# Optimization experiments

Hardware: AMD Instinct MI355X
Metric: run time of the kernel (lower is better)

## Reference

```python
import jax, jax.numpy as jnp
import numpy as np

N_NODES = 100000
N_EDGES = 600000
F_IN = 128
F_OUT = 128


def setup_inputs() -> dict:
    key = jax.random.key(0)
    ks = jax.random.split(key, 9)
    stdv = 1.0 / np.sqrt(F_OUT)
    return {
        "x": jax.random.normal(ks[0], (N_NODES, F_IN), dtype=jnp.float32),
        "weight": jax.random.uniform(ks[1], (F_IN, F_OUT), dtype=jnp.float32, minval=-stdv, maxval=stdv),
        "bias": jax.random.uniform(ks[2], (F_OUT,), dtype=jnp.float32, minval=-stdv, maxval=stdv),
        "vals0": jax.random.uniform(ks[3], (N_EDGES,), dtype=jnp.float32),
        "vals1": jax.random.uniform(ks[4], (N_EDGES,), dtype=jnp.float32),
        "rows0": jax.random.randint(ks[5], (N_EDGES,), 0, N_NODES, dtype=jnp.int32),
        "cols0": jax.random.randint(ks[6], (N_EDGES,), 0, N_NODES, dtype=jnp.int32),
        "rows1": jax.random.randint(ks[7], (N_EDGES,), 0, N_NODES, dtype=jnp.int32),
        "cols1": jax.random.randint(ks[8], (N_EDGES,), 0, N_NODES, dtype=jnp.int32),
    }


def _spmm(rows, cols, vals, dense, n):
    # COO sparse [n,n] @ dense [n,f]: gather source rows, scale, scatter-add to dest rows
    msgs = dense[cols] * vals[:, None]          # [E, f]
    return jax.ops.segment_sum(msgs, rows, num_segments=n)


def reference(x, weight, bias, vals0, vals1, rows0, cols0, rows1, cols1):
    n = x.shape[0]
    support = x @ weight                         # [N, F_OUT] dense GEMM
    out = _spmm(rows0, cols0, vals0, support, n) \
        + _spmm(rows1, cols1, vals1, support, n)
    return out + bias
```

## Files before the change

### kernel.cpp

```cpp
#include <hip/hip_runtime.h>


#define FDIM 128
#define EPB 2048

typedef __attribute__((ext_vector_type(8))) short short8;
typedef __attribute__((ext_vector_type(4))) float floatx4;

__device__ __forceinline__ unsigned short f32_to_bf16(float f) {
    unsigned int u = __float_as_uint(f);
    unsigned int r = u + 0x7fffu + ((u >> 16) & 1u);
    return (unsigned short)(r >> 16);
}

__device__ __forceinline__ float bf16_lo(unsigned int u) {
    return __uint_as_float((u & 0xffffu) << 16);
}
__device__ __forceinline__ float bf16_hi(unsigned int u) {
    return __uint_as_float(u & 0xffff0000u);
}

__global__ __launch_bounds__(256) void wt_conv(const float* __restrict__ w,
                                               unsigned short* __restrict__ wt) {
    int idx = blockIdx.x * 256 + threadIdx.x;
    int nn = idx >> 7, k = idx & 127;
    wt[idx] = f32_to_bf16(w[(size_t)k * FDIM + nn]);
}

__global__ __launch_bounds__(256) void gemm_reg(const float* __restrict__ x,
                                                const unsigned short* __restrict__ wt,
                                                unsigned short* __restrict__ support,
                                                int n) {
    const int tid = threadIdx.x;
    const int wv = tid >> 6, lane = tid & 63;
    const int quad = lane >> 4, lr = lane & 15;
    const int row0 = (blockIdx.x * 4 + wv) * 16;
    if (row0 >= n) return;

    short8 b[8][4];
    #pragma unroll
    for (int nt = 0; nt < 8; ++nt)
        #pragma unroll
        for (int ks = 0; ks < 4; ++ks)
            b[nt][ks] = *(const short8*)(wt + (size_t)(nt * 16 + lr) * FDIM + ks * 32 + quad * 8);

    floatx4 acc[8];
    #pragma unroll
    for (int nt = 0; nt < 8; ++nt) acc[nt] = (floatx4)0.f;

    const int arow = row0 + lr;
    const bool rowok = arow < n;
    const float* xr = x + (size_t)arow * FDIM;

    float4 f[8];
    #pragma unroll
    for (int ks = 0; ks < 4; ++ks) {
        f[2 * ks]     = rowok ? *(const float4*)(xr + ks * 32 + quad * 8)     : make_float4(0.f,0.f,0.f,0.f);
        f[2 * ks + 1] = rowok ? *(const float4*)(xr + ks * 32 + quad * 8 + 4) : make_float4(0.f,0.f,0.f,0.f);
    }

    #pragma unroll
    for (int ks = 0; ks < 4; ++ks) {
        float4 lo = f[2 * ks], hi = f[2 * ks + 1];
        short8 a;
        a[0] = (short)f32_to_bf16(lo.x); a[1] = (short)f32_to_bf16(lo.y);
        a[2] = (short)f32_to_bf16(lo.z); a[3] = (short)f32_to_bf16(lo.w);
        a[4] = (short)f32_to_bf16(hi.x); a[5] = (short)f32_to_bf16(hi.y);
        a[6] = (short)f32_to_bf16(hi.z); a[7] = (short)f32_to_bf16(hi.w);
        #pragma unroll
        for (int nt = 0; nt < 8; ++nt)
            acc[nt] = __builtin_amdgcn_mfma_f32_16x16x32_bf16(a, b[nt][ks], acc[nt], 0, 0, 0);
    }

    #pragma unroll
    for (int i = 0; i < 4; ++i) {
        int row = row0 + quad * 4 + i;
        if (row < n) {
            #pragma unroll
            for (int nt = 0; nt < 8; ++nt)
                support[(size_t)row * FDIM + nt * 16 + lr] = f32_to_bf16(acc[nt][i]);
        }
    }
}

__global__ __launch_bounds__(256) void hist_rows(const int* __restrict__ rows0,
                                                 const int* __restrict__ rows1,
                                                 int* __restrict__ count,
                                                 int* __restrict__ rank, int E) {
    int gid = blockIdx.x * 256 + threadIdx.x;
    if (gid >= 2 * E) return;
    int r = (gid < E) ? rows0[gid] : rows1[gid - E];
    rank[gid] = atomicAdd(&count[r], 1);
}

__device__ __forceinline__ int block_incl_scan(int v, int tid, int* lds) {
    int lane = tid & 63, wv = tid >> 6;
    #pragma unroll
    for (int d = 1; d < 64; d <<= 1) {
        int y = __shfl_up(v, d);
        if (lane >= d) v += y;
    }
    if (lane == 63) lds[wv] = v;
    __syncthreads();
    if (wv == 0 && lane < 4) {
        int s = lds[lane];
        #pragma unroll
        for (int d = 1; d < 4; d <<= 1) {
            int y = __shfl_up(s, d);
            if (lane >= d) s += y;
        }
        lds[4 + lane] = s;
    }
    __syncthreads();
    int add = (wv > 0) ? lds[4 + wv - 1] : 0;
    return v + add;
}

__global__ __launch_bounds__(256) void rowptr_scan(const int* __restrict__ count,
                                                   int* __restrict__ rowptr,
                                                   int* __restrict__ gcur, int n) {
    __shared__ int lds[8];
    __shared__ int base;
    int tid = threadIdx.x;
    int idx = blockIdx.x * 256 + tid;
    int v = (idx < n) ? count[idx] : 0;
    int inc = block_incl_scan(v, tid, lds);
    if (tid == 255) base = atomicAdd(gcur, inc);
    __syncthreads();
    if (idx < n) rowptr[idx] = base + inc - v;
}

__global__ __launch_bounds__(256) void compute_pos(const int* __restrict__ rows0,
                                                   const int* __restrict__ rows1,
                                                   const int* __restrict__ rank,
                                                   const int* __restrict__ rowptr,
                                                   int* __restrict__ pos, int E) {
    int gid = blockIdx.x * 256 + threadIdx.x;
    if (gid >= 2 * E) return;
    int r = (gid < E) ? rows0[gid] : rows1[gid - E];
    pos[gid] = rowptr[r] + rank[gid];
}

__global__ __launch_bounds__(256) void scatter_pos(
    const int* __restrict__ cols0, const float* __restrict__ vals0,
    const int* __restrict__ cols1, const float* __restrict__ vals1,
    const int* __restrict__ pos,
    int2* __restrict__ rec, int E, int psize) {
    const int p = blockIdx.x & 7;
    const int base = (blockIdx.x >> 3) * EPB;
    const int tid = threadIdx.x;
    #pragma unroll
    for (int it = 0; it < EPB / 256; ++it) {
        int gid = base + it * 256 + tid;
        if (gid < 2 * E) {
            int pv = pos[gid];
            if (pv / psize == p) {
                int c; float v;
                if (gid < E) { c = cols0[gid]; v = vals0[gid]; }
                else         { int e = gid - E; c = cols1[e]; v = vals1[e]; }
                rec[pv] = make_int2(c, __float_as_int(v));
            }
        }
    }
}

__global__ __launch_bounds__(256) void pull_csr(const unsigned short* __restrict__ support,
                                                const int* __restrict__ rowptr,
                                                const int* __restrict__ count,
                                                const int2* __restrict__ rec,
                                                const float* __restrict__ bias,
                                                float* __restrict__ out, int n) {
    int wid = (blockIdx.x * 256 + threadIdx.x) >> 6;
    int lane = threadIdx.x & 63;
    if (wid >= n) return;
    int beg = rowptr[wid];
    int end = beg + count[wid];
    float ax = 0.f, ay = 0.f;
    const char* sp = (const char*)support;
    const unsigned loff = (unsigned)lane << 2;

    for (int base = beg; base < end; base += 64) {
        int m = end - base; if (m > 64) m = 64;
        long long pk = 0;
        if (lane < m) pk = *(const long long*)&rec[base + lane];
        int j = 0;
        for (; j + 8 <= m; j += 8) {
            long long p0 = __shfl(pk, j);
            long long p1 = __shfl(pk, j + 1);
            long long p2 = __shfl(pk, j + 2);
            long long p3 = __shfl(pk, j + 3);
            long long p4 = __shfl(pk, j + 4);
            long long p5 = __shfl(pk, j + 5);
            long long p6 = __shfl(pk, j + 6);
            long long p7 = __shfl(pk, j + 7);
            unsigned u0 = *(const unsigned*)(sp + (((unsigned)p0) << 8) + loff);
            unsigned u1 = *(const unsigned*)(sp + (((unsigned)p1) << 8) + loff);
            unsigned u2 = *(const unsigned*)(sp + (((unsigned)p2) << 8) + loff);
            unsigned u3 = *(const unsigned*)(sp + (((unsigned)p3) << 8) + loff);
            unsigned u4 = *(const unsigned*)(sp + (((unsigned)p4) << 8) + loff);
            unsigned u5 = *(const unsigned*)(sp + (((unsigned)p5) << 8) + loff);
            unsigned u6 = *(const unsigned*)(sp + (((unsigned)p6) << 8) + loff);
            unsigned u7 = *(const unsigned*)(sp + (((unsigned)p7) << 8) + loff);
            float v0 = __int_as_float((int)(p0 >> 32));
            float v1 = __int_as_float((int)(p1 >> 32));
            float v2 = __int_as_float((int)(p2 >> 32));
            float v3 = __int_as_float((int)(p3 >> 32));
            float v4 = __int_as_float((int)(p4 >> 32));
            float v5 = __int_as_float((int)(p5 >> 32));
            float v6 = __int_as_float((int)(p6 >> 32));
            float v7 = __int_as_float((int)(p7 >> 32));
            ax += v0 * bf16_lo(u0); ay += v0 * bf16_hi(u0);
            ax += v1 * bf16_lo(u1); ay += v1 * bf16_hi(u1);
            ax += v2 * bf16_lo(u2); ay += v2 * bf16_hi(u2);
            ax += v3 * bf16_lo(u3); ay += v3 * bf16_hi(u3);
            ax += v4 * bf16_lo(u4); ay += v4 * bf16_hi(u4);
            ax += v5 * bf16_lo(u5); ay += v5 * bf16_hi(u5);
            ax += v6 * bf16_lo(u6); ay += v6 * bf16_hi(u6);
            ax += v7 * bf16_lo(u7); ay += v7 * bf16_hi(u7);
        }
        for (; j + 4 <= m; j += 4) {
            long long p0 = __shfl(pk, j);
            long long p1 = __shfl(pk, j + 1);
            long long p2 = __shfl(pk, j + 2);
            long long p3 = __shfl(pk, j + 3);
            unsigned u0 = *(const unsigned*)(sp + (((unsigned)p0) << 8) + loff);
            unsigned u1 = *(const unsigned*)(sp + (((unsigned)p1) << 8) + loff);
            unsigned u2 = *(const unsigned*)(sp + (((unsigned)p2) << 8) + loff);
            unsigned u3 = *(const unsigned*)(sp + (((unsigned)p3) << 8) + loff);
            float v0 = __int_as_float((int)(p0 >> 32));
            float v1 = __int_as_float((int)(p1 >> 32));
            float v2 = __int_as_float((int)(p2 >> 32));
            float v3 = __int_as_float((int)(p3 >> 32));
            ax += v0 * bf16_lo(u0); ay += v0 * bf16_hi(u0);
            ax += v1 * bf16_lo(u1); ay += v1 * bf16_hi(u1);
            ax += v2 * bf16_lo(u2); ay += v2 * bf16_hi(u2);
            ax += v3 * bf16_lo(u3); ay += v3 * bf16_hi(u3);
        }
        for (; j < m; ++j) {
            long long p = __shfl(pk, j);
            unsigned u = *(const unsigned*)(sp + (((unsigned)p) << 8) + loff);
            float v = __int_as_float((int)(p >> 32));
            ax += v * bf16_lo(u); ay += v * bf16_hi(u);
        }
    }
    float2 b = *(const float2*)(bias + lane * 2);
    *(float2*)(out + (size_t)wid * FDIM + lane * 2) = make_float2(ax + b.x, ay + b.y);
}

__global__ __launch_bounds__(256) void init_bias(const float* __restrict__ bias,
                                                 float* __restrict__ out, int n) {
    int idx = blockIdx.x * 256 + threadIdx.x;
    int total = n * (FDIM / 4);
    if (idx < total) {
        int j = (idx & (FDIM / 4 - 1)) * 4;
        float4 b = *(const float4*)(bias + j);
        *(float4*)(out + (size_t)idx * 4) = b;
    }
}

__global__ __launch_bounds__(256) void scatter_bf16(
    const unsigned short* __restrict__ support,
    const int* __restrict__ rows0, const int* __restrict__ cols0, const float* __restrict__ vals0,
    const int* __restrict__ rows1, const int* __restrict__ cols1, const float* __restrict__ vals1,
    float* __restrict__ out, int E) {
    int gid = blockIdx.x * 256 + threadIdx.x;
    int lane = gid & 63;
    int eg = gid >> 6;
    if (eg >= 2 * E) return;
    int r, c; float v;
    if (eg < E) { r = rows0[eg]; c = cols0[eg]; v = vals0[eg]; }
    else        { int e = eg - E; r = rows1[e]; c = cols1[e]; v = vals1[e]; }
    unsigned int u = *(const unsigned int*)(support + (size_t)c * FDIM + lane * 2);
    float sx = bf16_lo(u);
    float sy = bf16_hi(u);
    float* op = out + (size_t)r * FDIM + lane * 2;
    atomicAdd(op,     sx * v);
    atomicAdd(op + 1, sy * v);
}

static inline size_t align256(size_t v) { return (v + 255) & ~(size_t)255; }

extern "C" void kernel_launch(void* const* d_in, const int* in_sizes, int n_in,
                              void* d_out, int out_size, void* d_ws, size_t ws_size,
                              hipStream_t stream) {
    const float* x     = (const float*)d_in[0];
    const float* w     = (const float*)d_in[1];
    const float* bias  = (const float*)d_in[2];
    const float* vals0 = (const float*)d_in[3];
    const float* vals1 = (const float*)d_in[4];
    const int*   rows0 = (const int*)d_in[5];
    const int*   cols0 = (const int*)d_in[6];
    const int*   rows1 = (const int*)d_in[7];
    const int*   cols1 = (const int*)d_in[8];
    const int n = in_sizes[0] / FDIM;
    const int E = in_sizes[3];
    float* out = (float*)d_out;

    const int NB = (n + 255) / 256;

    size_t off = 0;
    unsigned short* support = (unsigned short*)((char*)d_ws + off);
    off = align256(off + (size_t)n * FDIM * 2);
    unsigned short* wt = (unsigned short*)((char*)d_ws + off);
    off = align256(off + (size_t)FDIM * FDIM * 2);
    size_t count_off = off;
    int*  count  = (int*)((char*)d_ws + off);  off = align256(off + (size_t)n * 4);
    int*  gcur   = (int*)((char*)d_ws + off);  off = align256(off + 4);
    size_t zero_bytes = off - count_off;
    int*  rowptr = (int*)((char*)d_ws + off);  off = align256(off + (size_t)n * 4);
    int*  rank   = (int*)((char*)d_ws + off);  off = align256(off + (size_t)2 * E * 4);
    int*  pos    = (int*)((char*)d_ws + off);  off = align256(off + (size_t)2 * E * 4);
    int2* rec    = (int2*)((char*)d_ws + off); off = align256(off + (size_t)2 * E * 8);

    wt_conv<<<(FDIM * FDIM) / 256, 256, 0, stream>>>(w, wt);
    gemm_reg<<<(n + 63) / 64, 256, 0, stream>>>(x, wt, support, n);

    if (off <= ws_size) {
        hipMemsetAsync((char*)d_ws + count_off, 0, zero_bytes, stream);
        int eb = (2 * E + 255) / 256;
        hist_rows<<<eb, 256, 0, stream>>>(rows0, rows1, count, rank, E);
        rowptr_scan<<<NB, 256, 0, stream>>>(count, rowptr, gcur, n);
        compute_pos<<<eb, 256, 0, stream>>>(rows0, rows1, rank, rowptr, pos, E);
        int psize = (2 * E + 7) / 8;
        int ntiles = (2 * E + EPB - 1) / EPB;
        scatter_pos<<<ntiles * 8, 256, 0, stream>>>(cols0, vals0, cols1, vals1,
                                                    pos, rec, E, psize);
        pull_csr<<<(n + 3) / 4, 256, 0, stream>>>(support, rowptr, count, rec, bias, out, n);
    } else {
        int total4 = n * (FDIM / 4);
        init_bias<<<(total4 + 255) / 256, 256, 0, stream>>>(bias, out, n);
        long long tthreads = 2LL * E * 64;
        int blocks = (int)((tthreads + 255) / 256);
        scatter_bf16<<<blocks, 256, 0, stream>>>(support, rows0, cols0, vals0,
                                                 rows1, cols1, vals1, out, E);
    }
}
```

Before: 291.7 us.

## Fuse launches: merge weight prep with memset, GEMM with histogram, drop pos pass

Weight transpose/convert and the count zeroing now share one prep kernel, replacing a separate memset. The histogram blocks are appended to the GEMM grid, so the atomic counting runs alongside the MFMA work, and each GEMM wave now handles four 16-row tiles so the B fragments loaded into registers are reused. The compute_pos kernel and the pos array are removed: the scatter partitions by row and computes the destination from rowptr and rank directly. This cuts kernel launches and one full pass over the edges, at the cost of extra gathers in the scatter and a GEMM grid with fewer blocks.

```diff
diff --git a/kernel.cpp b/kernel.cpp
--- a/kernel.cpp
+++ b/kernel.cpp
@@ -20,22 +20,42 @@
     return __uint_as_float(u & 0xffff0000u);
 }
 
-__global__ __launch_bounds__(256) void wt_conv(const float* __restrict__ w,
-                                               unsigned short* __restrict__ wt) {
-    int idx = blockIdx.x * 256 + threadIdx.x;
-    int nn = idx >> 7, k = idx & 127;
-    wt[idx] = f32_to_bf16(w[(size_t)k * FDIM + nn]);
-}
-
-__global__ __launch_bounds__(256) void gemm_reg(const float* __restrict__ x,
-                                                const unsigned short* __restrict__ wt,
-                                                unsigned short* __restrict__ support,
-                                                int n) {
+__global__ __launch_bounds__(256) void prep(const float* __restrict__ w,
+                                            unsigned short* __restrict__ wt,
+                                            int* __restrict__ zero_ptr, int zero_ints) {
+    int bid = blockIdx.x;
+    if (bid < 64) {
+        int idx = bid * 256 + threadIdx.x;
+        int nn = idx >> 7, k = idx & 127;
+        wt[idx] = f32_to_bf16(w[(size_t)k * FDIM + nn]);
+    } else {
+        int idx = (bid - 64) * 256 + threadIdx.x;
+        if (idx < zero_ints) zero_ptr[idx] = 0;
+    }
+}
+
+__global__ __launch_bounds__(256) void gemm_hist(const float* __restrict__ x,
+                                                 const unsigned short* __restrict__ wt,
+                                                 unsigned short* __restrict__ support,
+                                                 int n,
+                                                 const int* __restrict__ rows0,
+                                                 const int* __restrict__ rows1,
+                                                 int* __restrict__ count,
+                                                 int* __restrict__ rank,
+                                                 int E, int GB) {
+    if ((int)blockIdx.x >= GB) {
+        int gid = (blockIdx.x - GB) * 256 + threadIdx.x;
+        if (gid < 2 * E) {
+            int r = (gid < E) ? rows0[gid] : rows1[gid - E];
+            rank[gid] = atomicAdd(&count[r], 1);
+        }
+        return;
+    }
     const int tid = threadIdx.x;
     const int wv = tid >> 6, lane = tid & 63;
     const int quad = lane >> 4, lr = lane & 15;
-    const int row0 = (blockIdx.x * 4 + wv) * 16;
-    if (row0 >= n) return;
+    const int rbase = blockIdx.x * 256 + wv * 64;
+    if (rbase >= n) return;
 
     short8 b[8][4];
     #pragma unroll
@@ -44,53 +64,41 @@
         for (int ks = 0; ks < 4; ++ks)
             b[nt][ks] = *(const short8*)(wt + (size_t)(nt * 16 + lr) * FDIM + ks * 32 + quad * 8);
 
-    floatx4 acc[8];
-    #pragma unroll
-    for (int nt = 0; nt < 8; ++nt) acc[nt] = (floatx4)0.f;
-
-    const int arow = row0 + lr;
-    const bool rowok = arow < n;
-    const float* xr = x + (size_t)arow * FDIM;
-
-    float4 f[8];
-    #pragma unroll
-    for (int ks = 0; ks < 4; ++ks) {
-        f[2 * ks]     = rowok ? *(const float4*)(xr + ks * 32 + quad * 8)     : make_float4(0.f,0.f,0.f,0.f);
-        f[2 * ks + 1] = rowok ? *(const float4*)(xr + ks * 32 + quad * 8 + 4) : make_float4(0.f,0.f,0.f,0.f);
-    }
-
-    #pragma unroll
-    for (int ks = 0; ks < 4; ++ks) {
-        float4 lo = f[2 * ks], hi = f[2 * ks + 1];
-        short8 a;
-        a[0] = (short)f32_to_bf16(lo.x); a[1] = (short)f32_to_bf16(lo.y);
-        a[2] = (short)f32_to_bf16(lo.z); a[3] = (short)f32_to_bf16(lo.w);
-        a[4] = (short)f32_to_bf16(hi.x); a[5] = (short)f32_to_bf16(hi.y);
-        a[6] = (short)f32_to_bf16(hi.z); a[7] = (short)f32_to_bf16(hi.w);
-        #pragma unroll
-        for (int nt = 0; nt < 8; ++nt)
-            acc[nt] = __builtin_amdgcn_mfma_f32_16x16x32_bf16(a, b[nt][ks], acc[nt], 0, 0, 0);
-    }
-
-    #pragma unroll
-    for (int i = 0; i < 4; ++i) {
-        int row = row0 + quad * 4 + i;
-        if (row < n) {
+    for (int t = 0; t < 4; ++t) {
+        const int row0 = rbase + t * 16;
+        if (row0 >= n) break;
+        const int arow = row0 + lr;
+        const bool rowok = arow < n;
+        const float* xr = x + (size_t)arow * FDIM;
+
+        floatx4 acc[8];
+        #pragma unroll
+        for (int nt = 0; nt < 8; ++nt) acc[nt] = (floatx4)0.f;
+
+        #pragma unroll
+        for (int ks = 0; ks < 4; ++ks) {
+            float4 lo = rowok ? *(const float4*)(xr + ks * 32 + quad * 8)     : make_float4(0.f,0.f,0.f,0.f);
+            float4 hi = rowok ? *(const float4*)(xr + ks * 32 + quad * 8 + 4) : make_float4(0.f,0.f,0.f,0.f);
+            short8 a;
+            a[0] = (short)f32_to_bf16(lo.x); a[1] = (short)f32_to_bf16(lo.y);
+            a[2] = (short)f32_to_bf16(lo.z); a[3] = (short)f32_to_bf16(lo.w);
+            a[4] = (short)f32_to_bf16(hi.x); a[5] = (short)f32_to_bf16(hi.y);
+            a[6] = (short)f32_to_bf16(hi.z); a[7] = (short)f32_to_bf16(hi.w);
             #pragma unroll
             for (int nt = 0; nt < 8; ++nt)
-                support[(size_t)row * FDIM + nt * 16 + lr] = f32_to_bf16(acc[nt][i]);
-        }
-    }
-}
-
-__global__ __launch_bounds__(256) void hist_rows(const int* __restrict__ rows0,
-                                                 const int* __restrict__ rows1,
-                                                 int* __restrict__ count,
-                                                 int* __restrict__ rank, int E) {
-    int gid = blockIdx.x * 256 + threadIdx.x;
-    if (gid >= 2 * E) return;
-    int r = (gid < E) ? rows0[gid] : rows1[gid - E];
-    rank[gid] = atomicAdd(&count[r], 1);
+                acc[nt] = __builtin_amdgcn_mfma_f32_16x16x32_bf16(a, b[nt][ks], acc[nt], 0, 0, 0);
+        }
+
+        #pragma unroll
+        for (int i = 0; i < 4; ++i) {
+            int row = row0 + quad * 4 + i;
+            if (row < n) {
+                #pragma unroll
+                for (int nt = 0; nt < 8; ++nt)
+                    support[(size_t)row * FDIM + nt * 16 + lr] = f32_to_bf16(acc[nt][i]);
+            }
+        }
+    }
 }
 
 __device__ __forceinline__ int block_incl_scan(int v, int tid, int* lds) {
@@ -130,22 +138,11 @@
     if (idx < n) rowptr[idx] = base + inc - v;
 }
 
-__global__ __launch_bounds__(256) void compute_pos(const int* __restrict__ rows0,
-                                                   const int* __restrict__ rows1,
-                                                   const int* __restrict__ rank,
-                                                   const int* __restrict__ rowptr,
-                                                   int* __restrict__ pos, int E) {
-    int gid = blockIdx.x * 256 + threadIdx.x;
-    if (gid >= 2 * E) return;
-    int r = (gid < E) ? rows0[gid] : rows1[gid - E];
-    pos[gid] = rowptr[r] + rank[gid];
-}
-
-__global__ __launch_bounds__(256) void scatter_pos(
-    const int* __restrict__ cols0, const float* __restrict__ vals0,
-    const int* __restrict__ cols1, const float* __restrict__ vals1,
-    const int* __restrict__ pos,
-    int2* __restrict__ rec, int E, int psize) {
+__global__ __launch_bounds__(256) void scatter_row(
+    const int* __restrict__ rows0, const int* __restrict__ cols0, const float* __restrict__ vals0,
+    const int* __restrict__ rows1, const int* __restrict__ cols1, const float* __restrict__ vals1,
+    const int* __restrict__ rank, const int* __restrict__ rowptr,
+    int2* __restrict__ rec, int E, int nper) {
     const int p = blockIdx.x & 7;
     const int base = (blockIdx.x >> 3) * EPB;
     const int tid = threadIdx.x;
@@ -153,12 +150,12 @@
     for (int it = 0; it < EPB / 256; ++it) {
         int gid = base + it * 256 + tid;
         if (gid < 2 * E) {
-            int pv = pos[gid];
-            if (pv / psize == p) {
+            int r = (gid < E) ? rows0[gid] : rows1[gid - E];
+            if (r / nper == p) {
                 int c; float v;
                 if (gid < E) { c = cols0[gid]; v = vals0[gid]; }
                 else         { int e = gid - E; c = cols1[e]; v = vals1[e]; }
-                rec[pv] = make_int2(c, __float_as_int(v));
+                rec[rowptr[r] + rank[gid]] = make_int2(c, __float_as_int(v));
             }
         }
     }
@@ -309,22 +306,26 @@
     size_t zero_bytes = off - count_off;
     int*  rowptr = (int*)((char*)d_ws + off);  off = align256(off + (size_t)n * 4);
     int*  rank   = (int*)((char*)d_ws + off);  off = align256(off + (size_t)2 * E * 4);
-    int*  pos    = (int*)((char*)d_ws + off);  off = align256(off + (size_t)2 * E * 4);
     int2* rec    = (int2*)((char*)d_ws + off); off = align256(off + (size_t)2 * E * 8);
 
-    wt_conv<<<(FDIM * FDIM) / 256, 256, 0, stream>>>(w, wt);
-    gemm_reg<<<(n + 63) / 64, 256, 0, stream>>>(x, wt, support, n);
-
-    if (off <= ws_size) {
-        hipMemsetAsync((char*)d_ws + count_off, 0, zero_bytes, stream);
-        int eb = (2 * E + 255) / 256;
-        hist_rows<<<eb, 256, 0, stream>>>(rows0, rows1, count, rank, E);
+    const bool fits = off <= ws_size;
+    const int GB = (n + 255) / 256;
+    const int HB = fits ? (2 * E + 255) / 256 : 0;
+
+    int zero_ints = fits ? (int)(zero_bytes / 4) : 0;
+    int zb = (zero_ints + 255) / 256;
+    prep<<<64 + zb, 256, 0, stream>>>(w, wt, (int*)((char*)d_ws + count_off), zero_ints);
+
+    gemm_hist<<<GB + HB, 256, 0, stream>>>(x, wt, support, n,
+                                           rows0, rows1, count, rank, E, GB);
+
+    if (fits) {
         rowptr_scan<<<NB, 256, 0, stream>>>(count, rowptr, gcur, n);
-        compute_pos<<<eb, 256, 0, stream>>>(rows0, rows1, rank, rowptr, pos, E);
-        int psize = (2 * E + 7) / 8;
+        int nper = (n + 7) / 8;
         int ntiles = (2 * E + EPB - 1) / EPB;
-        scatter_pos<<<ntiles * 8, 256, 0, stream>>>(cols0, vals0, cols1, vals1,
-                                                    pos, rec, E, psize);
+        scatter_row<<<ntiles * 8, 256, 0, stream>>>(rows0, cols0, vals0,
+                                                    rows1, cols1, vals1,
+                                                    rank, rowptr, rec, E, nper);
         pull_csr<<<(n + 3) / 4, 256, 0, stream>>>(support, rowptr, count, rec, bias, out, n);
     } else {
         int total4 = n * (FDIM / 4);
```

Result: faster. 264.4 us (-9.3%).
